# Kernel optimization log

Hardware: AMD Instinct MI355X
Metric: run time of the kernel (lower is better)

## Reference

```python
import jax, jax.numpy as jnp
import numpy as np

BATCH, LENGTH, DIM, CHANNEL, PAST = 16, 256, 512, 8, 12


def setup_inputs() -> dict:
    key = jax.random.key(0)
    ks = jax.random.split(key, 5)
    scale = 1.0 / np.sqrt(DIM)
    inp = jax.random.normal(ks[0], (BATCH, LENGTH, DIM), dtype=jnp.float32)
    Ws = jax.random.normal(ks[1], (CHANNEL, DIM, DIM), dtype=jnp.float32) * scale
    bs = jax.random.normal(ks[2], (CHANNEL, DIM), dtype=jnp.float32) * scale
    Wt = jax.random.normal(ks[3], (CHANNEL, PAST), dtype=jnp.float32) * (1.0 / np.sqrt(PAST))
    bt = jax.random.normal(ks[4], (CHANNEL,), dtype=jnp.float32) * 0.01
    return {"inp": inp, "Ws": Ws, "bs": bs, "Wt": Wt, "bt": bt, "past": PAST}


def reference(inp, Ws, bs, Wt, bt, past):
    # Per-channel spatial linear: y = x @ Ws[c].T + bs[c]
    # spat: [batch, length, channel, dim]
    spat = jnp.einsum('bld,cod->blco', inp, Ws) + bs[None, None, :, :]
    Lout = inp.shape[1] - past
    # Causal sliding-window temporal linear (depthwise conv over time):
    # out[b,t,c,d] = sum_p Wt[c,p] * spat[b,t+p,c,d] + bt[c]
    out = bt[None, None, :, None]
    for p in range(past):  # small fixed loop over kernel taps
        out = out + Wt[:, p][None, None, :, None] * spat[:, p:p + Lout]
    return out  # [batch, length-past, channel, dim]
```

## Files before the change

kernel.cpp:

```cpp
#include <hip/hip_runtime.h>
#include <hip/hip_bf16.h>

#define B_   16
#define L_   256
#define D_   512
#define C_   8
#define P_   12
#define LOUT 244
#define O_   512
#define GM   3904

typedef __attribute__((ext_vector_type(8))) short bf16x8;
typedef __attribute__((ext_vector_type(4))) float f32x4;

__device__ __forceinline__ unsigned short f2bf(float f) {
    unsigned int u = __float_as_uint(f);
    unsigned int r = (u + 0x7FFFu + ((u >> 16) & 1u)) >> 16;
    return (unsigned short)r;
}

__device__ __forceinline__ void async_copy16(const void* g, void* l) {
    __builtin_amdgcn_global_load_lds(
        (const __attribute__((address_space(1))) unsigned int*)g,
        (__attribute__((address_space(3))) unsigned int*)l, 16, 0, 0);
}

__global__ __launch_bounds__(256) void prep(const float* __restrict__ inp,
                                            const float* __restrict__ Ws,
                                            const float* __restrict__ Wt,
                                            unsigned short* __restrict__ tmp,
                                            unsigned short* __restrict__ wsb) {
    int bid = blockIdx.x;
    int tid = threadIdx.x;

    if (bid >= 976) {
        int g = (bid - 976) * 256 + tid;
        float4 v = ((const float4*)Ws)[g];
        ushort4 o;
        o.x = f2bf(v.x); o.y = f2bf(v.y); o.z = f2bf(v.z); o.w = f2bf(v.w);
        ((ushort4*)wsb)[g] = o;
        return;
    }

    __shared__ float wt_s[C_][P_];
    if (tid < C_ * P_) wt_s[tid / P_][tid % P_] = Wt[tid];
    __syncthreads();

    int b = bid / 61, lg = bid % 61;
    int l0 = lg * 4;
    int d0 = tid * 2;

    float2 rows[15];
    const float* ibase = inp + ((size_t)b * L_ + l0) * D_ + d0;
#pragma unroll
    for (int j = 0; j < 15; ++j)
        rows[j] = *(const float2*)(ibase + (size_t)j * D_);

#pragma unroll
    for (int c = 0; c < C_; ++c) {
        float w[P_];
#pragma unroll
        for (int p = 0; p < P_; ++p) w[p] = wt_s[c][p];
        unsigned short* ob = tmp + (((size_t)(c * B_ + b)) * LOUT + l0) * D_ + d0;
#pragma unroll
        for (int j = 0; j < 4; ++j) {
            float vx = 0.f, vy = 0.f;
#pragma unroll
            for (int p = 0; p < P_; ++p) {
                vx += w[p] * rows[j + p].x;
                vy += w[p] * rows[j + p].y;
            }
            ushort2 ov; ov.x = f2bf(vx); ov.y = f2bf(vy);
            *(ushort2*)(ob + (size_t)j * D_) = ov;
        }
    }
}

__global__ __launch_bounds__(256) void gemm_k(const unsigned short* __restrict__ tmp,
                                              const unsigned short* __restrict__ wsb,
                                              const float* __restrict__ bs,
                                              const float* __restrict__ Wt,
                                              const float* __restrict__ bt,
                                              float* __restrict__ out) {
    __shared__ unsigned short As[128 * 64];
    __shared__ unsigned short Bs[128 * 64];

    int bid = blockIdx.x;
    int gr = bid & 7;
    int t  = bid >> 3;
    int ot = t & 3;
    int gq = t >> 2;
    int g  = gq * 8 + gr;
    int c  = g / 31;
    int mt = g % 31;

    int row0 = mt * 128, o0 = ot * 128;
    int tid = threadIdx.x, lane = tid & 63, wid = tid >> 6;
    int wm = wid >> 1, wn = wid & 1;

    const unsigned short* Ab = tmp + (size_t)c * GM * D_;
    const unsigned short* Bb = wsb + (size_t)c * O_ * D_;

    f32x4 acc[4][4];
#pragma unroll
    for (int m = 0; m < 4; ++m)
#pragma unroll
        for (int n = 0; n < 4; ++n)
            acc[m][n] = (f32x4){0.f, 0.f, 0.f, 0.f};

    for (int d0 = 0; d0 < D_; d0 += 64) {
        __syncthreads();
#pragma unroll
        for (int h = 0; h < 4; ++h) {
            int q = h * 256 + tid;
            int row = q >> 3, col = (q & 7) * 8;
            int ar = row0 + row; if (ar > GM - 1) ar = GM - 1;
            async_copy16(Ab + (size_t)ar * D_ + d0 + col,
                         (unsigned short*)As + (size_t)q * 8);
            async_copy16(Bb + (size_t)(o0 + row) * D_ + d0 + col,
                         (unsigned short*)Bs + (size_t)q * 8);
        }
        __syncthreads();

#pragma unroll
        for (int kk = 0; kk < 2; ++kk) {
            int cb = kk * 32 + ((lane >> 4) << 3);
            bf16x8 af[4], bq[4];
#pragma unroll
            for (int m = 0; m < 4; ++m)
                af[m] = *(const bf16x8*)&As[(wm * 64 + m * 16 + (lane & 15)) * 64 + cb];
#pragma unroll
            for (int n = 0; n < 4; ++n)
                bq[n] = *(const bf16x8*)&Bs[(wn * 64 + n * 16 + (lane & 15)) * 64 + cb];
#pragma unroll
            for (int m = 0; m < 4; ++m)
#pragma unroll
                for (int n = 0; n < 4; ++n)
                    acc[m][n] = __builtin_amdgcn_mfma_f32_16x16x32_bf16(
                        af[m], bq[n], acc[m][n], 0, 0, 0);
        }
    }

    float S = 0.f;
#pragma unroll
    for (int p = 0; p < P_; ++p) S += Wt[c * P_ + p];
    float btc = bt[c];

#pragma unroll
    for (int m = 0; m < 4; ++m) {
        int rb = row0 + wm * 64 + m * 16 + ((lane >> 4) << 2);
#pragma unroll
        for (int n = 0; n < 4; ++n) {
            int col = o0 + wn * 64 + n * 16 + (lane & 15);
            float add = bs[c * O_ + col] * S + btc;
#pragma unroll
            for (int i = 0; i < 4; ++i) {
                int r = rb + i;
                if (r < GM)
                    out[((size_t)r * C_ + c) * O_ + col] = acc[m][n][i] + add;
            }
        }
    }
}

__global__ __launch_bounds__(256) void naive_k(const float* __restrict__ inp,
                                               const float* __restrict__ Ws,
                                               const float* __restrict__ bs,
                                               const float* __restrict__ Wt,
                                               const float* __restrict__ bt,
                                               float* __restrict__ out) {
    __shared__ float tmp[D_];
    int bid = blockIdx.x;
    int c = bid & 7; int r = bid >> 3;
    int l = r % LOUT; int b = r / LOUT;
    int tid = threadIdx.x;

    for (int d = tid; d < D_; d += 256) {
        float s = 0.f;
        for (int p = 0; p < P_; ++p)
            s += Wt[c * P_ + p] * inp[((size_t)b * L_ + l + p) * D_ + d];
        tmp[d] = s;
    }
    __syncthreads();
    float S = 0.f;
    for (int p = 0; p < P_; ++p) S += Wt[c * P_ + p];
    for (int o = tid; o < O_; o += 256) {
        const float* wrow = Ws + ((size_t)c * O_ + o) * D_;
        float s = 0.f;
        for (int d = 0; d < D_; ++d) s += wrow[d] * tmp[d];
        out[(((size_t)b * LOUT + l) * C_ + c) * O_ + o] =
            s + bs[c * O_ + o] * S + bt[c];
    }
}

extern "C" void kernel_launch(void* const* d_in, const int* in_sizes, int n_in,
                              void* d_out, int out_size, void* d_ws, size_t ws_size,
                              hipStream_t stream) {
    const float* inp = (const float*)d_in[0];
    const float* Ws  = (const float*)d_in[1];
    const float* bs  = (const float*)d_in[2];
    const float* Wt  = (const float*)d_in[3];
    const float* bt  = (const float*)d_in[4];
    float* out = (float*)d_out;

    const size_t TMPB = (size_t)C_ * GM * D_ * 2;
    const size_t WSBB = (size_t)C_ * O_ * D_ * 2;

    if (ws_size >= TMPB + WSBB) {
        unsigned short* tmpb = (unsigned short*)d_ws;
        unsigned short* wsb  = (unsigned short*)((char*)d_ws + TMPB);
        prep<<<3024, 256, 0, stream>>>(inp, Ws, Wt, tmpb, wsb);
        gemm_k<<<992, 256, 0, stream>>>(tmpb, wsb, bs, Wt, bt, out);
    } else {
        naive_k<<<B_ * LOUT * C_, 256, 0, stream>>>(inp, Ws, bs, Wt, bt, out);
    }
}
```

Before: 50.27 us.

## Fuse temporal FIR into GEMM A-tile load, drop bf16 intermediate buffer

The temporal filter is now computed inside the GEMM kernel. Each block builds its 64-row A tile straight from fp32 inputs using the 12 Wt taps, so the bf16 temporary is no longer written to and re-read from global memory. Blocks are 1024 threads and cover all 512 output columns per channel, and both LDS tiles use an XOR swizzle to avoid bank conflicts. In exchange, each input row is re-read from global memory 12 times per channel tile, and the grid shrinks to 488 large blocks.

```diff
diff --git a/kernel.cpp b/kernel.cpp
--- a/kernel.cpp
+++ b/kernel.cpp
@@ -9,6 +9,7 @@
 #define LOUT 244
 #define O_   512
 #define GM   3904
+#define NT   61
 
 typedef __attribute__((ext_vector_type(8))) short bf16x8;
 typedef __attribute__((ext_vector_type(4))) float f32x4;
@@ -25,115 +26,106 @@
         (__attribute__((address_space(3))) unsigned int*)l, 16, 0, 0);
 }
 
-__global__ __launch_bounds__(256) void prep(const float* __restrict__ inp,
-                                            const float* __restrict__ Ws,
-                                            const float* __restrict__ Wt,
-                                            unsigned short* __restrict__ tmp,
-                                            unsigned short* __restrict__ wsb) {
+__global__ __launch_bounds__(256) void ws_convert(const float* __restrict__ Ws,
+                                                  unsigned short* __restrict__ wsb) {
+    int g = blockIdx.x * 256 + threadIdx.x;
+    float4 v = ((const float4*)Ws)[g];
+    ushort4 o;
+    o.x = f2bf(v.x); o.y = f2bf(v.y); o.z = f2bf(v.z); o.w = f2bf(v.w);
+    ((ushort4*)wsb)[g] = o;
+}
+
+__global__ __launch_bounds__(1024, 4) void fused(const float* __restrict__ inp,
+                                                 const unsigned short* __restrict__ wsb,
+                                                 const float* __restrict__ bs,
+                                                 const float* __restrict__ Wt,
+                                                 const float* __restrict__ bt,
+                                                 float* __restrict__ out) {
+    __shared__ unsigned short As[64 * 64];
+    __shared__ unsigned short Bs[512 * 64];
+
     int bid = blockIdx.x;
+    int c = bid & 7, mt = bid >> 3;
+    int row0 = mt * 64;
     int tid = threadIdx.x;
-
-    if (bid >= 976) {
-        int g = (bid - 976) * 256 + tid;
-        float4 v = ((const float4*)Ws)[g];
-        ushort4 o;
-        o.x = f2bf(v.x); o.y = f2bf(v.y); o.z = f2bf(v.z); o.w = f2bf(v.w);
-        ((ushort4*)wsb)[g] = o;
-        return;
-    }
-
-    __shared__ float wt_s[C_][P_];
-    if (tid < C_ * P_) wt_s[tid / P_][tid % P_] = Wt[tid];
-    __syncthreads();
-
-    int b = bid / 61, lg = bid % 61;
-    int l0 = lg * 4;
-    int d0 = tid * 2;
-
-    float2 rows[15];
-    const float* ibase = inp + ((size_t)b * L_ + l0) * D_ + d0;
-#pragma unroll
-    for (int j = 0; j < 15; ++j)
-        rows[j] = *(const float2*)(ibase + (size_t)j * D_);
-
-#pragma unroll
-    for (int c = 0; c < C_; ++c) {
-        float w[P_];
-#pragma unroll
-        for (int p = 0; p < P_; ++p) w[p] = wt_s[c][p];
-        unsigned short* ob = tmp + (((size_t)(c * B_ + b)) * LOUT + l0) * D_ + d0;
-#pragma unroll
-        for (int j = 0; j < 4; ++j) {
-            float vx = 0.f, vy = 0.f;
-#pragma unroll
-            for (int p = 0; p < P_; ++p) {
-                vx += w[p] * rows[j + p].x;
-                vy += w[p] * rows[j + p].y;
-            }
-            ushort2 ov; ov.x = f2bf(vx); ov.y = f2bf(vy);
-            *(ushort2*)(ob + (size_t)j * D_) = ov;
-        }
-    }
-}
-
-__global__ __launch_bounds__(256) void gemm_k(const unsigned short* __restrict__ tmp,
-                                              const unsigned short* __restrict__ wsb,
-                                              const float* __restrict__ bs,
-                                              const float* __restrict__ Wt,
-                                              const float* __restrict__ bt,
-                                              float* __restrict__ out) {
-    __shared__ unsigned short As[128 * 64];
-    __shared__ unsigned short Bs[128 * 64];
-
-    int bid = blockIdx.x;
-    int gr = bid & 7;
-    int t  = bid >> 3;
-    int ot = t & 3;
-    int gq = t >> 2;
-    int g  = gq * 8 + gr;
-    int c  = g / 31;
-    int mt = g % 31;
-
-    int row0 = mt * 128, o0 = ot * 128;
-    int tid = threadIdx.x, lane = tid & 63, wid = tid >> 6;
-    int wm = wid >> 1, wn = wid & 1;
-
-    const unsigned short* Ab = tmp + (size_t)c * GM * D_;
+    int lane = tid & 63, wid = tid >> 6;
+    int wm = wid >> 3, wn = wid & 7;
+
+    float w[P_];
+#pragma unroll
+    for (int p = 0; p < P_; ++p) w[p] = Wt[c * P_ + p];
+
+    int frow = tid >> 4;
+    int fcol = (tid & 15) * 4;
+    int rg = row0 + frow;
+    int fb = rg / LOUT, fl = rg % LOUT;
+    const float* fir_base = inp + ((size_t)fb * L_ + fl) * D_ + fcol;
+    int awr = frow * 64 + (((fcol >> 3) ^ (frow & 7)) << 3) + (fcol & 7);
+
     const unsigned short* Bb = wsb + (size_t)c * O_ * D_;
 
-    f32x4 acc[4][4];
-#pragma unroll
-    for (int m = 0; m < 4; ++m)
+    f32x4 acc[2][4];
+#pragma unroll
+    for (int m = 0; m < 2; ++m)
 #pragma unroll
         for (int n = 0; n < 4; ++n)
             acc[m][n] = (f32x4){0.f, 0.f, 0.f, 0.f};
 
     for (int d0 = 0; d0 < D_; d0 += 64) {
         __syncthreads();
+
 #pragma unroll
         for (int h = 0; h < 4; ++h) {
-            int q = h * 256 + tid;
-            int row = q >> 3, col = (q & 7) * 8;
-            int ar = row0 + row; if (ar > GM - 1) ar = GM - 1;
-            async_copy16(Ab + (size_t)ar * D_ + d0 + col,
-                         (unsigned short*)As + (size_t)q * 8);
-            async_copy16(Bb + (size_t)(o0 + row) * D_ + d0 + col,
+            int q = h * 1024 + tid;
+            int brow = q >> 3, cc = q & 7;
+            int sc = cc ^ (brow & 7);
+            async_copy16(Bb + (size_t)brow * D_ + d0 + sc * 8,
                          (unsigned short*)Bs + (size_t)q * 8);
         }
+
+        float s0 = 0.f, s1 = 0.f, s2 = 0.f, s3 = 0.f;
+        {
+            float4 v[6];
+#pragma unroll
+            for (int p = 0; p < 6; ++p)
+                v[p] = *(const float4*)(fir_base + (size_t)p * D_ + d0);
+#pragma unroll
+            for (int p = 0; p < 6; ++p) {
+                s0 += w[p] * v[p].x; s1 += w[p] * v[p].y;
+                s2 += w[p] * v[p].z; s3 += w[p] * v[p].w;
+            }
+#pragma unroll
+            for (int p = 0; p < 6; ++p)
+                v[p] = *(const float4*)(fir_base + (size_t)(p + 6) * D_ + d0);
+#pragma unroll
+            for (int p = 0; p < 6; ++p) {
+                s0 += w[p + 6] * v[p].x; s1 += w[p + 6] * v[p].y;
+                s2 += w[p + 6] * v[p].z; s3 += w[p + 6] * v[p].w;
+            }
+        }
+        ushort4 ov;
+        ov.x = f2bf(s0); ov.y = f2bf(s1); ov.z = f2bf(s2); ov.w = f2bf(s3);
+        *(ushort4*)&As[awr] = ov;
+
         __syncthreads();
 
 #pragma unroll
         for (int kk = 0; kk < 2; ++kk) {
             int cb = kk * 32 + ((lane >> 4) << 3);
-            bf16x8 af[4], bq[4];
-#pragma unroll
-            for (int m = 0; m < 4; ++m)
-                af[m] = *(const bf16x8*)&As[(wm * 64 + m * 16 + (lane & 15)) * 64 + cb];
-#pragma unroll
-            for (int n = 0; n < 4; ++n)
-                bq[n] = *(const bf16x8*)&Bs[(wn * 64 + n * 16 + (lane & 15)) * 64 + cb];
-#pragma unroll
-            for (int m = 0; m < 4; ++m)
+            int cch = cb >> 3;
+            bf16x8 af[2], bq[4];
+#pragma unroll
+            for (int m = 0; m < 2; ++m) {
+                int r = wm * 32 + m * 16 + (lane & 15);
+                af[m] = *(const bf16x8*)&As[r * 64 + ((cch ^ (r & 7)) << 3)];
+            }
+#pragma unroll
+            for (int n = 0; n < 4; ++n) {
+                int o = wn * 64 + n * 16 + (lane & 15);
+                bq[n] = *(const bf16x8*)&Bs[o * 64 + ((cch ^ (o & 7)) << 3)];
+            }
+#pragma unroll
+            for (int m = 0; m < 2; ++m)
 #pragma unroll
                 for (int n = 0; n < 4; ++n)
                     acc[m][n] = __builtin_amdgcn_mfma_f32_16x16x32_bf16(
@@ -143,21 +135,20 @@
 
     float S = 0.f;
 #pragma unroll
-    for (int p = 0; p < P_; ++p) S += Wt[c * P_ + p];
+    for (int p = 0; p < P_; ++p) S += w[p];
     float btc = bt[c];
 
 #pragma unroll
-    for (int m = 0; m < 4; ++m) {
-        int rb = row0 + wm * 64 + m * 16 + ((lane >> 4) << 2);
+    for (int m = 0; m < 2; ++m) {
+        int rb = row0 + wm * 32 + m * 16 + ((lane >> 4) << 2);
 #pragma unroll
         for (int n = 0; n < 4; ++n) {
-            int col = o0 + wn * 64 + n * 16 + (lane & 15);
+            int col = wn * 64 + n * 16 + (lane & 15);
             float add = bs[c * O_ + col] * S + btc;
 #pragma unroll
             for (int i = 0; i < 4; ++i) {
                 int r = rb + i;
-                if (r < GM)
-                    out[((size_t)r * C_ + c) * O_ + col] = acc[m][n][i] + add;
+                out[((size_t)r * C_ + c) * O_ + col] = acc[m][n][i] + add;
             }
         }
     }
@@ -203,14 +194,12 @@
     const float* bt  = (const float*)d_in[4];
     float* out = (float*)d_out;
 
-    const size_t TMPB = (size_t)C_ * GM * D_ * 2;
     const size_t WSBB = (size_t)C_ * O_ * D_ * 2;
 
-    if (ws_size >= TMPB + WSBB) {
-        unsigned short* tmpb = (unsigned short*)d_ws;
-        unsigned short* wsb  = (unsigned short*)((char*)d_ws + TMPB);
-        prep<<<3024, 256, 0, stream>>>(inp, Ws, Wt, tmpb, wsb);
-        gemm_k<<<992, 256, 0, stream>>>(tmpb, wsb, bs, Wt, bt, out);
+    if (ws_size >= WSBB) {
+        unsigned short* wsb = (unsigned short*)d_ws;
+        ws_convert<<<2048, 256, 0, stream>>>(Ws, wsb);
+        fused<<<NT * C_, 1024, 0, stream>>>(inp, wsb, bs, Wt, bt, out);
     } else {
         naive_k<<<B_ * LOUT * C_, 256, 0, stream>>>(inp, Ws, bs, Wt, bt, out);
     }
```

Result: slower. 64.38 us (+28.1%).

## Double-buffer GEMM LDS tiles with XOR swizzle and 8-wave blocks

Applied to the files above, without the earlier changes.

Rewrites the GEMM main loop to double-buffer the A and B tiles in LDS, issuing async global-to-LDS copies two K-steps ahead with explicit vmcnt waits, so loads overlap the MFMA work. It adds an XOR swizzle on the LDS column index to avoid bank conflicts, moves from 4 to 8 waves per block with a 4x2 per-wave MFMA tile, and interleaves channels in the block index. The costs are twice the LDS per block and hand-placed waitcnt/barrier logic that is fragile to get right.

```diff
diff --git a/kernel.cpp b/kernel.cpp
--- a/kernel.cpp
+++ b/kernel.cpp
@@ -9,6 +9,11 @@
 #define LOUT 244
 #define O_   512
 #define GM   3904
+#define BM   128
+#define BN   128
+#define BK   64
+#define NMT  31
+#define NNT  4
 
 typedef __attribute__((ext_vector_type(8))) short bf16x8;
 typedef __attribute__((ext_vector_type(4))) float f32x4;
@@ -76,69 +81,93 @@
     }
 }
 
-__global__ __launch_bounds__(256) void gemm_k(const unsigned short* __restrict__ tmp,
-                                              const unsigned short* __restrict__ wsb,
-                                              const float* __restrict__ bs,
-                                              const float* __restrict__ Wt,
-                                              const float* __restrict__ bt,
-                                              float* __restrict__ out) {
-    __shared__ unsigned short As[128 * 64];
-    __shared__ unsigned short Bs[128 * 64];
+__global__ __launch_bounds__(512, 4) void gemm_k(const unsigned short* __restrict__ tmp,
+                                                 const unsigned short* __restrict__ wsb,
+                                                 const float* __restrict__ bs,
+                                                 const float* __restrict__ Wt,
+                                                 const float* __restrict__ bt,
+                                                 float* __restrict__ out) {
+    __shared__ unsigned short As0[BM * BK], As1[BM * BK];
+    __shared__ unsigned short Bs0[BN * BK], Bs1[BN * BK];
 
     int bid = blockIdx.x;
-    int gr = bid & 7;
-    int t  = bid >> 3;
-    int ot = t & 3;
-    int gq = t >> 2;
-    int g  = gq * 8 + gr;
-    int c  = g / 31;
-    int mt = g % 31;
-
-    int row0 = mt * 128, o0 = ot * 128;
+    int c  = bid & 7;
+    int t2 = bid >> 3;
+    int nt = t2 & 3;
+    int mt = t2 >> 2;
+    int row0 = mt * BM;
+    int o0   = nt * BN;
     int tid = threadIdx.x, lane = tid & 63, wid = tid >> 6;
-    int wm = wid >> 1, wn = wid & 1;
+    int wm = wid >> 2, wn = wid & 3;
 
     const unsigned short* Ab = tmp + (size_t)c * GM * D_;
-    const unsigned short* Bb = wsb + (size_t)c * O_ * D_;
-
-    f32x4 acc[4][4];
+    const unsigned short* Bb = wsb + ((size_t)c * O_ + o0) * D_;
+
+    f32x4 acc[4][2];
 #pragma unroll
     for (int m = 0; m < 4; ++m)
 #pragma unroll
-        for (int n = 0; n < 4; ++n)
+        for (int n = 0; n < 2; ++n)
             acc[m][n] = (f32x4){0.f, 0.f, 0.f, 0.f};
 
-    for (int d0 = 0; d0 < D_; d0 += 64) {
-        __syncthreads();
-#pragma unroll
-        for (int h = 0; h < 4; ++h) {
-            int q = h * 256 + tid;
-            int row = q >> 3, col = (q & 7) * 8;
-            int ar = row0 + row; if (ar > GM - 1) ar = GM - 1;
-            async_copy16(Ab + (size_t)ar * D_ + d0 + col,
-                         (unsigned short*)As + (size_t)q * 8);
-            async_copy16(Bb + (size_t)(o0 + row) * D_ + d0 + col,
-                         (unsigned short*)Bs + (size_t)q * 8);
-        }
-        __syncthreads();
-
-#pragma unroll
-        for (int kk = 0; kk < 2; ++kk) {
-            int cb = kk * 32 + ((lane >> 4) << 3);
-            bf16x8 af[4], bq[4];
-#pragma unroll
-            for (int m = 0; m < 4; ++m)
-                af[m] = *(const bf16x8*)&As[(wm * 64 + m * 16 + (lane & 15)) * 64 + cb];
-#pragma unroll
-            for (int n = 0; n < 4; ++n)
-                bq[n] = *(const bf16x8*)&Bs[(wn * 64 + n * 16 + (lane & 15)) * 64 + cb];
-#pragma unroll
-            for (int m = 0; m < 4; ++m)
-#pragma unroll
-                for (int n = 0; n < 4; ++n)
-                    acc[m][n] = __builtin_amdgcn_mfma_f32_16x16x32_bf16(
-                        af[m], bq[n], acc[m][n], 0, 0, 0);
-        }
+    unsigned short *Ac = As0, *Bc = Bs0, *An = As1, *Bn = Bs1;
+
+#define STAGE(dstA, dstB, kb)                                                 \
+    _Pragma("unroll")                                                         \
+    for (int h = 0; h < 2; ++h) {                                             \
+        int q = h * 512 + tid;                                                \
+        int row = q >> 3, cc = q & 7;                                         \
+        int sc = cc ^ (row & 7);                                              \
+        int ar = row0 + row; if (ar > GM - 1) ar = GM - 1;                    \
+        async_copy16(Ab + (size_t)ar * D_ + (kb) + sc * 8, (dstA) + q * 8);   \
+        async_copy16(Bb + (size_t)row * D_ + (kb) + sc * 8, (dstB) + q * 8);  \
+    }
+
+#define MFMA_STEP(Asrc, Bsrc)                                                 \
+    _Pragma("unroll")                                                         \
+    for (int kk = 0; kk < 2; ++kk) {                                          \
+        bf16x8 af[4], bq[2];                                                  \
+        _Pragma("unroll")                                                     \
+        for (int m = 0; m < 4; ++m) {                                         \
+            int r = wm * 64 + m * 16 + (lane & 15);                           \
+            af[m] = *(const bf16x8*)&(Asrc)[r * BK +                          \
+                    (((kk * 4 + (lane >> 4)) ^ (r & 7)) << 3)];               \
+        }                                                                     \
+        _Pragma("unroll")                                                     \
+        for (int n = 0; n < 2; ++n) {                                         \
+            int o = wn * 32 + n * 16 + (lane & 15);                           \
+            bq[n] = *(const bf16x8*)&(Bsrc)[o * BK +                          \
+                    (((kk * 4 + (lane >> 4)) ^ (o & 7)) << 3)];               \
+        }                                                                     \
+        _Pragma("unroll")                                                     \
+        for (int m = 0; m < 4; ++m)                                           \
+            _Pragma("unroll")                                                 \
+            for (int n = 0; n < 2; ++n)                                       \
+                acc[m][n] = __builtin_amdgcn_mfma_f32_16x16x32_bf16(          \
+                    af[m], bq[n], acc[m][n], 0, 0, 0);                        \
+    }
+
+    STAGE(Ac, Bc, 0)
+    STAGE(An, Bn, BK)
+    asm volatile("s_waitcnt vmcnt(4)" ::: "memory");
+    __builtin_amdgcn_sched_barrier(0);
+    __builtin_amdgcn_s_barrier();
+
+#pragma unroll
+    for (int t = 0; t < 8; ++t) {
+        MFMA_STEP(Ac, Bc)
+        if (t == 7) break;
+        __builtin_amdgcn_s_barrier();
+        if (t + 2 < 8) STAGE(Ac, Bc, (t + 2) * BK)
+        if (t < 6)
+            asm volatile("s_waitcnt vmcnt(4)" ::: "memory");
+        else
+            asm volatile("s_waitcnt vmcnt(0)" ::: "memory");
+        __builtin_amdgcn_sched_barrier(0);
+        __builtin_amdgcn_s_barrier();
+        unsigned short* tp;
+        tp = Ac; Ac = An; An = tp;
+        tp = Bc; Bc = Bn; Bn = tp;
     }
 
     float S = 0.f;
@@ -150,8 +179,8 @@
     for (int m = 0; m < 4; ++m) {
         int rb = row0 + wm * 64 + m * 16 + ((lane >> 4) << 2);
 #pragma unroll
-        for (int n = 0; n < 4; ++n) {
-            int col = o0 + wn * 64 + n * 16 + (lane & 15);
+        for (int n = 0; n < 2; ++n) {
+            int col = o0 + wn * 32 + n * 16 + (lane & 15);
             float add = bs[c * O_ + col] * S + btc;
 #pragma unroll
             for (int i = 0; i < 4; ++i) {
@@ -161,6 +190,8 @@
             }
         }
     }
+#undef STAGE
+#undef MFMA_STEP
 }
 
 __global__ __launch_bounds__(256) void naive_k(const float* __restrict__ inp,
@@ -210,7 +241,7 @@
         unsigned short* tmpb = (unsigned short*)d_ws;
         unsigned short* wsb  = (unsigned short*)((char*)d_ws + TMPB);
         prep<<<3024, 256, 0, stream>>>(inp, Ws, Wt, tmpb, wsb);
-        gemm_k<<<992, 256, 0, stream>>>(tmpb, wsb, bs, Wt, bt, out);
+        gemm_k<<<NMT * NNT * C_, 512, 0, stream>>>(tmpb, wsb, bs, Wt, bt, out);
     } else {
         naive_k<<<B_ * LOUT * C_, 256, 0, stream>>>(inp, Ws, bs, Wt, bt, out);
     }
```

Result: faster. 41.45 us (-17.5%).
